# Kernel optimization log

Hardware: AMD Instinct MI355X
Metric: run time of the kernel (lower is better)

## Reference

```python
import jax, jax.numpy as jnp
import numpy as np
from jax import lax

N = 2; C_IN = 256
H0, W0 = 100, 152
H1, W1 = 50, 76
DYN_CH = 34            # 4 init_offset + 4 bound_pt_offset + 18 semantic_pt_offset + 8 reg_aggr_attn
REG_CH = 4             # 4 boundary points x 1 channel each
NUM_CLASSES = 80
SEM_PTS = 9
CLS_CH = SEM_PTS * NUM_CLASSES
BOUND_PTS = 4
RATIO = 0.5            # LIMIT_BOUND_POINT_OFFSET_RATIO

_BASE = np.array([[1,0,0,0],[0,1,0,0],[0.5,0,0.5,0],
                  [0,0.5,0,0.5],[0,0,1,0],[0,0,0,1]], np.float32)
BOUND_MAT = jnp.asarray(_BASE[[0,3,2,1,4,3,2,5]])                      # (8,4) box -> cross-shaped 4 pts
SEM_MAT = jnp.asarray(_BASE[[0,1,0,3,0,5,2,1,2,3,2,5,4,1,4,3,4,5]])    # (18,4) box -> 3x3 pts
BOUND_OFF_IDX = jnp.array([1, 2, 5, 6])   # tangential coordinate channel of each boundary point
LOC_IDX = jnp.array([0, 3, 4, 7])         # box-side coordinate channel of each boundary point

def conv3x3(x, w, b):
    y = lax.conv_general_dilated(x, w, (1, 1), 'SAME',
                                 dimension_numbers=('NCHW', 'OIHW', 'NCHW'))
    return y + b[None, :, None, None]

def conv1x1(x, w):
    return jnp.einsum('oi,nihw->nohw', w[:, :, 0, 0], x)

def pred_collect(fmap, pts, point_num, reduce_points, bias=None):
    # Bilinearly sample per-point channel groups of fmap at dynamic point locations.
    # fmap: (N, P*c, Hm, Wm); pts: (N, 2P, H, W) with (x, y) pairs per point.
    Nb, C, Hm, Wm = fmap.shape
    P = point_num; c = C // P
    H, W = pts.shape[2], pts.shape[3]
    fm = fmap.reshape(Nb, P, c, Hm, Wm)
    pg = pts.reshape(Nb, P, 2, H, W)
    def sample(f, pt):  # f: (c, Hm, Wm), pt: (2, H, W)
        x = jnp.clip(pt[0], 0.0, Wm - 1.0)
        y = jnp.clip(pt[1], 0.0, Hm - 1.0)
        x0 = jnp.floor(x); y0 = jnp.floor(y)
        fx = x - x0; fy = y - y0
        x0i = x0.astype(jnp.int32); y0i = y0.astype(jnp.int32)
        x1i = jnp.minimum(x0i + 1, Wm - 1); y1i = jnp.minimum(y0i + 1, Hm - 1)
        v00 = f[:, y0i, x0i]; v01 = f[:, y0i, x1i]
        v10 = f[:, y1i, x0i]; v11 = f[:, y1i, x1i]
        return v00*(1-fx)*(1-fy) + v01*fx*(1-fy) + v10*(1-fx)*fy + v11*fx*fy
    vals = jax.vmap(jax.vmap(sample))(fm, pg)  # (N, P, c, H, W)
    if reduce_points:
        out = vals.sum(axis=1)
        if bias is not None:
            out = out + bias[None, :, None, None]
        return out
    return vals.reshape(Nb, P * c, H, W)

def head_forward(reg_feats, cls_feats, anchors, dyn_w, dyn_b, reg_w, cls_w, cls_b):
    reg_maps = [conv1x1(x, reg_w) for x in reg_feats]
    cls_maps = [conv1x1(x, cls_w) for x in cls_feats]
    cls_scores, coarse_boxes, reg_boxes = [], [], []
    for i, (reg_feat, anchor) in enumerate(zip(reg_feats, anchors)):
        Nb, _, H, W = reg_feat.shape
        pred = conv3x3(reg_feat, dyn_w, dyn_b)
        init_off, bpt_off, spt_off, attn = jnp.split(pred, [4, 8, 26], axis=1)
        coarse = anchor + init_off                                  # (N,4,H,W) = (x1,y1,x2,y2)
        # straight-through clamp of boundary-point tangential offsets to +-wh/2*ratio
        bpt_off = bpt_off.reshape(Nb, 2, 2, 1, H, W)
        wh = jnp.stack([coarse[:, 3] - coarse[:, 1],
                        coarse[:, 2] - coarse[:, 0]], axis=1) / 2 * RATIO  # (N,2,H,W) [h,w]
        thres = wh[:, None, :, None]                                # (N,1,2,1,H,W)
        extra = jnp.maximum(bpt_off - thres, 0.0) + jnp.minimum(bpt_off + thres, 0.0)
        bpt_off = (bpt_off - lax.stop_gradient(extra)).reshape(Nb, 4, H, W)
        bound_pt = lax.stop_gradient(jnp.einsum('oc,nchw->nohw', BOUND_MAT, coarse))
        bound_pt = bound_pt.at[:, BOUND_OFF_IDX].add(bpt_off)       # (N,8,H,W)
        bound_pt_loc = bound_pt[:, LOC_IDX]                         # (N,4,H,W)
        reg_val = pred_collect(reg_maps[i], bound_pt, BOUND_PTS, False)  # (N,4,H,W)
        if i > 0:
            attn_sm = jax.nn.softmax(attn.reshape(Nb, BOUND_PTS, 2, H, W), axis=2)
            reg_hi = reg_val.reshape(Nb, BOUND_PTS, 1, 1, H, W)
            reg_lo = pred_collect(reg_maps[i - 1], bound_pt * 2, BOUND_PTS, False)
            reg_lo = reg_lo.reshape(Nb, BOUND_PTS, 1, 1, H, W) * 0.5
            reg_val = (jnp.concatenate([reg_lo, reg_hi], axis=2)
                       * attn_sm[:, :, :, None]).sum(axis=2).reshape(Nb, -1, H, W)
        reg_box = (lax.stop_gradient(bound_pt_loc) + reg_val).reshape(Nb, 4, -1, H, W).mean(axis=2)
        sem_pt = lax.stop_gradient(jnp.einsum('oc,nchw->nohw', SEM_MAT, coarse)) + spt_off
        cls_score = pred_collect(cls_maps[i], sem_pt, SEM_PTS, True, cls_b)  # (N,80,H,W)
        cls_scores.append(cls_score); coarse_boxes.append(coarse); reg_boxes.append(reg_box)
    return cls_scores, coarse_boxes, reg_boxes

def make_anchor(H, W):
    gy, gx = jnp.meshgrid(jnp.arange(H, dtype=jnp.float32),
                          jnp.arange(W, dtype=jnp.float32), indexing='ij')
    a = jnp.stack([gx - 4.0, gy - 4.0, gx + 4.0, gy + 4.0], axis=0)
    return jnp.broadcast_to(a[None], (N, 4, H, W))

def setup_inputs() -> dict:
    key = jax.random.key(0)
    ks = jax.random.split(key, 7)
    return {
        "reg_feat0": jax.random.normal(ks[0], (N, C_IN, H0, W0), jnp.float32),
        "reg_feat1": jax.random.normal(ks[1], (N, C_IN, H1, W1), jnp.float32),
        "cls_feat0": jax.random.normal(ks[2], (N, C_IN, H0, W0), jnp.float32),
        "cls_feat1": jax.random.normal(ks[3], (N, C_IN, H1, W1), jnp.float32),
        "anchor0": make_anchor(H0, W0),
        "anchor1": make_anchor(H1, W1),
        "dyn_w": jax.random.normal(ks[4], (DYN_CH, C_IN, 3, 3), jnp.float32) * 0.01,
        "dyn_b": jnp.zeros((DYN_CH,), jnp.float32),
        "reg_w": jax.random.normal(ks[5], (REG_CH, C_IN, 1, 1), jnp.float32) * 0.05,
        "cls_w": jax.random.normal(ks[6], (CLS_CH, C_IN, 1, 1), jnp.float32) * 0.05,
        "cls_b": jnp.zeros((NUM_CLASSES,), jnp.float32),
    }

def reference(reg_feat0, reg_feat1, cls_feat0, cls_feat1, anchor0, anchor1,
              dyn_w, dyn_b, reg_w, cls_w, cls_b):
    cls_scores, coarse_boxes, reg_boxes = head_forward(
        [reg_feat0, reg_feat1], [cls_feat0, cls_feat1], [anchor0, anchor1],
        dyn_w, dyn_b, reg_w, cls_w, cls_b)
    return (*cls_scores, *coarse_boxes, *reg_boxes)
```

## Files before the change

kernel.cpp:

```cpp
#include <hip/hip_runtime.h>
#include <hip/hip_bf16.h>
#include <cstdint>

#define N_BATCH 2
#define C_IN 256
#define DYN_CH 34
#define CLS_CH 720
#define NUM_CLASSES 80
#define NCOMB 48

#define P0c 15200
#define P1c 3800
#define M0c 30400
#define M1c 7600
#define MT0c 119
#define MT1c 30
#define CT0c 475
#define CT1c 119

typedef __attribute__((ext_vector_type(8))) short short8;
typedef __attribute__((ext_vector_type(4))) float f32x4;

typedef const unsigned int __attribute__((address_space(1)))* gas1_t;
typedef unsigned int __attribute__((address_space(3)))* las3_t;

__device__ __forceinline__ void async_ld16(const void* g, void* l) {
  __builtin_amdgcn_global_load_lds((gas1_t)g, (las3_t)l, 16, 0, 0);
}

__global__ __launch_bounds__(256) void pack_feat(
    const float* __restrict__ cls0, const float* __restrict__ cls1,
    const float* __restrict__ reg0, const float* __restrict__ reg1,
    const float* __restrict__ cls_w, const float* __restrict__ dyn_w,
    const float* __restrict__ reg_w, __hip_bfloat16* __restrict__ a0,
    __hip_bfloat16* __restrict__ a1, __hip_bfloat16* __restrict__ r0,
    __hip_bfloat16* __restrict__ r1, __hip_bfloat16* __restrict__ bpack,
    __hip_bfloat16* __restrict__ wpack) {
  int b = blockIdx.x;
  if (b >= 2384) {
    b -= 2384;
    if (b < 90) {
      int u = b * 256 + threadIdx.x;
      if (u >= 9 * 32 * 80) return;
      int ntile = u / 2560;
      int rem = u % 2560;
      int kcg = rem / 80;
      int ochl = rem % 80;
      int och = ntile * 80 + ochl;
      const float* wr = cls_w + (size_t)och * C_IN + kcg * 8;
      __hip_bfloat16 tmp[8];
#pragma unroll
      for (int c = 0; c < 8; ++c) tmp[c] = __float2bfloat16(wr[c]);
      *(uint4*)(bpack + (size_t)u * 8) = *(const uint4*)tmp;
    } else {
      int u = (b - 90) * 256 + threadIdx.x;
      if (u >= 13824) return;
      int j = u / 768;
      int r = u % 768;
      int n = r / 16;
      int s = r % 16;
      int ku = j * 16 + (s ^ (n & 7));
      int k0 = ku * 8;
      int tap = k0 >> 8;
      int c0 = k0 & 255;
      __hip_bfloat16 tmp[8];
#pragma unroll
      for (int i = 0; i < 8; ++i) {
        int c = c0 + i;
        float v = 0.f;
        if (n < DYN_CH) v = dyn_w[((size_t)n * C_IN + c) * 9 + tap];
        else if (n < DYN_CH + 4 && tap == 4)
          v = reg_w[(size_t)(n - DYN_CH) * C_IN + c];
        tmp[i] = __float2bfloat16(v);
      }
      *(uint4*)(wpack + (size_t)u * 8) = *(const uint4*)tmp;
    }
    return;
  }
  int j = b & 7;
  int mtg = b >> 3;
  const float* src;
  __hip_bfloat16* dst;
  int P, Mtot, mtile;
  if (mtg < 119)      { src = cls0; dst = a0; P = P0c; Mtot = M0c; mtile = mtg; }
  else if (mtg < 149) { src = cls1; dst = a1; P = P1c; Mtot = M1c; mtile = mtg - 119; }
  else if (mtg < 268) { src = reg0; dst = r0; P = P0c; Mtot = M0c; mtile = mtg - 149; }
  else                { src = reg1; dst = r1; P = P1c; Mtot = M1c; mtile = mtg - 268; }
  int wave = threadIdx.x >> 6;
  int lane = threadIdx.x & 63;
  int kcg = j * 4 + wave;
  int c0 = kcg * 8;
  int m4 = mtile * 256 + lane * 4;
  uint4* du = (uint4*)dst + (size_t)mtile * 8192 + (size_t)kcg * 256 + lane * 4;
  if (m4 < Mtot) {
    int n = m4 / P;
    int p = m4 - n * P;
    const float* sp = src + ((size_t)n * C_IN + c0) * P + p;
    float4 f[8];
#pragma unroll
    for (int c = 0; c < 8; ++c) f[c] = *(const float4*)(sp + (size_t)c * P);
#pragma unroll
    for (int i = 0; i < 4; ++i) {
      union { uint4 u; __hip_bfloat16 h[8]; } o;
#pragma unroll
      for (int c = 0; c < 8; ++c) {
        float v = (i == 0) ? f[c].x : (i == 1) ? f[c].y : (i == 2) ? f[c].z : f[c].w;
        o.h[c] = __float2bfloat16(v);
      }
      du[i] = o.u;
    }
  } else {
    uint4 z = {0u, 0u, 0u, 0u};
#pragma unroll
    for (int i = 0; i < 4; ++i) du[i] = z;
  }
}

__global__ __launch_bounds__(512) void cls_gemm_mfma(
    const uint4* __restrict__ Ap0, const uint4* __restrict__ Ap1,
    const uint4* __restrict__ Bp, __hip_bfloat16* __restrict__ out0,
    __hip_bfloat16* __restrict__ out1) {
  __shared__ uint4 Bsh[2560];
  int bb = blockIdx.x;
  int g = bb & 7;
  int loc = bb >> 3;
  int lm = loc / 9;
  int ntile = loc - lm * 9;
  int mtile = g * 19 + lm;
  if (mtile >= MT0c + MT1c) return;
  int tid = threadIdx.x;
  int w = tid >> 6;
  int lane = tid & 63;
  int l15 = lane & 15;
  int kq = lane >> 4;

  const uint4* Ap;
  __hip_bfloat16* out;
  int Mtot;
  if (mtile < MT0c) { Ap = Ap0; out = out0; Mtot = M0c; }
  else              { mtile -= MT0c; Ap = Ap1; out = out1; Mtot = M1c; }

  const uint4* Ab = Ap + (size_t)mtile * 8192;
  const uint4* Bb = Bp + (size_t)ntile * 2560;

#pragma unroll
  for (int i = 0; i < 5; ++i)
    async_ld16(Bb + i * 512 + w * 64 + lane, &Bsh[i * 512 + w * 64]);
  __syncthreads();

  f32x4 acc[2][5];
#pragma unroll
  for (int i = 0; i < 2; ++i)
#pragma unroll
    for (int j = 0; j < 5; ++j) acc[i][j] = (f32x4)0.f;

  const uint4* Abase = Ab + kq * 256 + w * 32 + l15;
#pragma unroll 2
  for (int kb = 0; kb < 8; ++kb) {
    uint4 a[2];
#pragma unroll
    for (int mi = 0; mi < 2; ++mi) a[mi] = Abase[kb * 1024 + mi * 16];
    short8 b[5];
    const uint4* Br = &Bsh[kb * 320 + kq * 80 + l15];
#pragma unroll
    for (int ni = 0; ni < 5; ++ni) b[ni] = *(const short8*)&Br[ni * 16];
#pragma unroll
    for (int mi = 0; mi < 2; ++mi)
#pragma unroll
      for (int ni = 0; ni < 5; ++ni)
        acc[mi][ni] = __builtin_amdgcn_mfma_f32_16x16x32_bf16(
            b[ni], *(const short8*)&a[mi], acc[mi][ni], 0, 0, 0);
  }

  int gbase = mtile * 256 + w * 32;
#pragma unroll
  for (int mi = 0; mi < 2; ++mi) {
    int px = gbase + mi * 16 + l15;
    if (px >= Mtot) continue;
    __hip_bfloat16* orow = out + (size_t)px * CLS_CH + ntile * 80 + kq * 4;
#pragma unroll
    for (int ni = 0; ni < 5; ++ni) {
      union { uint2 u; __hip_bfloat16 h[4]; } o;
#pragma unroll
      for (int r = 0; r < 4; ++r) o.h[r] = __float2bfloat16(acc[mi][ni][r]);
      *(uint2*)(orow + ni * 16) = o.u;
    }
  }
}

__global__ __launch_bounds__(256) void dyn_reg_conv_mfma(
    const uint4* __restrict__ rp0, const uint4* __restrict__ rp1,
    const uint4* __restrict__ wp, float* __restrict__ part0,
    float* __restrict__ part1) {
  __shared__ uint4 Bs[768];
  int g = blockIdx.x & 7;
  int i = blockIdx.x >> 3;
  int cnt = 74 + (g < 2 ? 1 : 0);
  if (i >= cnt) return;
  int bx = g * 74 + (g < 2 ? g : 2) + i;
  int tid = threadIdx.x;
  int wave = tid >> 6;
  int lane = tid & 63;
  int l15 = lane & 15;
  int kq = lane >> 4;

  const uint4* rp;
  float* part;
  int Mtot, P, W, H;
  if (bx < CT0c) { rp = rp0; part = part0; Mtot = M0c; P = P0c; W = 152; H = 100; }
  else { bx -= CT0c; rp = rp1; part = part1; Mtot = M1c; P = P1c; W = 76; H = 50; }

  int m = bx * 64 + wave * 16 + l15;
  bool mval = (m < Mtot);
  int mc = mval ? m : 0;
  int n = mc / P;
  int rem = mc - n * P;
  int y = rem / W;
  int x = rem - y * W;

  f32x4 acc[3];
#pragma unroll
  for (int q = 0; q < 3; ++q) acc[q] = (f32x4)0.f;

  for (int j = 0; j < 18; ++j) {
    const uint4* wsrc = wp + (size_t)j * 768 + wave * 192;
#pragma unroll
    for (int q = 0; q < 3; ++q)
      async_ld16(wsrc + q * 64 + lane, &Bs[wave * 192 + q * 64]);

    int tap = j >> 1;
    int cb8 = (j & 1) * 16;
    int dy = tap / 3 - 1, dx = tap % 3 - 1;
    int sy = y + dy, sx = x + dx;
    bool val = mval && ((unsigned)sy < (unsigned)H) && ((unsigned)sx < (unsigned)W);
    int sm = m + dy * W + dx;
    int smc = val ? sm : 0;
    size_t tbase = (size_t)(smc >> 8) * 8192 + (smc & 255);
    uint4 a[4];
#pragma unroll
    for (int t = 0; t < 4; ++t) {
      uint4 v = {0u, 0u, 0u, 0u};
      if (val) v = rp[tbase + (size_t)(cb8 + t * 4 + kq) * 256];
      a[t] = v;
    }
    __syncthreads();
#pragma unroll
    for (int t = 0; t < 4; ++t) {
#pragma unroll
      for (int ni = 0; ni < 3; ++ni) {
        int nn = ni * 16 + l15;
        short8 bf = *(const short8*)&Bs[nn * 16 + ((t * 4 + kq) ^ (nn & 7))];
        acc[ni] = __builtin_amdgcn_mfma_f32_16x16x32_bf16(
            *(short8*)&a[t], bf, acc[ni], 0, 0, 0);
      }
    }
    __syncthreads();
  }

  int mrow = bx * 64 + wave * 16 + kq * 4;
#pragma unroll
  for (int r = 0; r < 4; ++r) {
    int mm = mrow + r;
    if (mm >= Mtot) continue;
    float* dst = part + (size_t)mm * NCOMB + l15;
#pragma unroll
    for (int ni = 0; ni < 3; ++ni) dst[ni * 16] = acc[ni][r];
  }
}

__device__ __forceinline__ float samp(const float* __restrict__ part,
                                      int nbase, int W, int H,
                                      float px, float py, int ch) {
  float xc = fminf(fmaxf(px, 0.f), (float)(W - 1));
  float yc = fminf(fmaxf(py, 0.f), (float)(H - 1));
  float x0f = floorf(xc), y0f = floorf(yc);
  float fx = xc - x0f, fy = yc - y0f;
  int x0 = (int)x0f, y0 = (int)y0f;
  int x1 = min(x0 + 1, W - 1), y1 = min(y0 + 1, H - 1);
  float v00 = part[(size_t)(nbase + y0 * W + x0) * NCOMB + ch];
  float v01 = part[(size_t)(nbase + y0 * W + x1) * NCOMB + ch];
  float v10 = part[(size_t)(nbase + y1 * W + x0) * NCOMB + ch];
  float v11 = part[(size_t)(nbase + y1 * W + x1) * NCOMB + ch];
  return v00 * (1.f - fx) * (1.f - fy) + v01 * fx * (1.f - fy) +
         v10 * (1.f - fx) * fy + v11 * fx * fy;
}

__global__ __launch_bounds__(64) void decode(
    const float* __restrict__ part0, const float* __restrict__ part1,
    const float* __restrict__ dyn_b, const float* __restrict__ anchor0,
    const float* __restrict__ anchor1, float* __restrict__ out_coarse0,
    float* __restrict__ out_coarse1, float* __restrict__ out_regbox0,
    float* __restrict__ out_regbox1, int4* __restrict__ sidx0,
    float4* __restrict__ swt0, int4* __restrict__ sidx1,
    float4* __restrict__ swt1) {
  int g = blockIdx.x & 7;
  int i = blockIdx.x >> 3;
  int cnt = 74 + (g < 2 ? 1 : 0);
  if (i >= cnt) return;
  int u = g * 74 + (g < 2 ? g : 2) + i;
  const float* part;
  const float* anchor;
  float* out_coarse;
  float* out_regbox;
  int4* sidx;
  float4* swt;
  int Mtot, H, W, P, level, m;
  if (u < 475) {
    part = part0; anchor = anchor0; out_coarse = out_coarse0;
    out_regbox = out_regbox0; sidx = sidx0; swt = swt0;
    Mtot = M0c; H = 100; W = 152; P = P0c; level = 0;
    m = u * 64 + threadIdx.x;
  } else {
    part = part1; anchor = anchor1; out_coarse = out_coarse1;
    out_regbox = out_regbox1; sidx = sidx1; swt = swt1;
    Mtot = M1c; H = 50; W = 76; P = P1c; level = 1;
    m = (u - 475) * 64 + threadIdx.x;
  }
  if (m >= Mtot) return;
  int n = m / P;
  int p = m - n * P;
  float pr[40];
  {
    const float4* q0 = (const float4*)(part + (size_t)m * NCOMB);
#pragma unroll
    for (int o4 = 0; o4 < 10; ++o4) {
      float4 a = q0[o4];
      pr[4 * o4 + 0] = a.x;
      pr[4 * o4 + 1] = a.y;
      pr[4 * o4 + 2] = a.z;
      pr[4 * o4 + 3] = a.w;
    }
#pragma unroll
    for (int o = 0; o < DYN_CH; ++o) pr[o] += dyn_b[o];
  }
  const float* an = anchor + (size_t)n * 4 * P + p;
  float cb[4];
#pragma unroll
  for (int k = 0; k < 4; ++k) cb[k] = an[(size_t)k * P] + pr[k];
  float* oc = out_coarse + (size_t)n * 4 * P + p;
#pragma unroll
  for (int k = 0; k < 4; ++k) oc[(size_t)k * P] = cb[k];

  float thr_y = (cb[3] - cb[1]) * 0.25f;
  float thr_x = (cb[2] - cb[0]) * 0.25f;
  float bo[4];
#pragma unroll
  for (int j = 0; j < 4; ++j) {
    float thr = (j & 1) ? thr_x : thr_y;
    float b = pr[4 + j];
    float extra = fmaxf(b - thr, 0.f) + fminf(b + thr, 0.f);
    bo[j] = b - extra;
  }
  float cx = 0.5f * (cb[0] + cb[2]);
  float cy = 0.5f * (cb[1] + cb[3]);
  float bp[8] = {cb[0], cy + bo[0], cx + bo[1], cb[1],
                 cb[2], cy + bo[2], cx + bo[3], cb[3]};

  int nbase = n * P;
  int nbaseLo = n * P0c;
  float rb[4];
#pragma unroll
  for (int pt = 0; pt < 4; ++pt) {
    float hi = samp(part, nbase, W, H, bp[2 * pt], bp[2 * pt + 1],
                    DYN_CH + pt);
    float val;
    if (level == 0) {
      val = hi;
    } else {
      float lo = 0.5f * samp(part0, nbaseLo, 152, 100, bp[2 * pt] * 2.f,
                             bp[2 * pt + 1] * 2.f, DYN_CH + pt);
      float e0 = pr[26 + 2 * pt], e1 = pr[26 + 2 * pt + 1];
      float mx = fmaxf(e0, e1);
      float w0 = expf(e0 - mx), w1 = expf(e1 - mx);
      val = (lo * w0 + hi * w1) / (w0 + w1);
    }
    rb[pt] = val;
  }
  float* orb = out_regbox + (size_t)n * 4 * P + p;
  orb[0] = bp[0] + rb[0];
  orb[(size_t)P] = bp[3] + rb[1];
  orb[(size_t)2 * P] = bp[4] + rb[2];
  orb[(size_t)3 * P] = bp[7] + rb[3];

  float sx[9] = {cb[0], cb[0], cb[0], cx, cx, cx, cb[2], cb[2], cb[2]};
  float sy[9] = {cb[1], cy, cb[3], cb[1], cy, cb[3], cb[1], cy, cb[3]};
#pragma unroll
  for (int k = 0; k < 9; ++k) {
    float px = sx[k] + pr[8 + 2 * k];
    float py = sy[k] + pr[8 + 2 * k + 1];
    float xc = fminf(fmaxf(px, 0.f), (float)(W - 1));
    float yc = fminf(fmaxf(py, 0.f), (float)(H - 1));
    float x0f = floorf(xc), y0f = floorf(yc);
    float fx = xc - x0f, fy = yc - y0f;
    int x0 = (int)x0f, y0 = (int)y0f;
    int x1 = min(x0 + 1, W - 1), y1 = min(y0 + 1, H - 1);
    int4 iv;
    iv.x = (nbase + y0 * W + x0) * CLS_CH + k * 80;
    iv.y = (x1 - x0) * CLS_CH;
    iv.z = (y1 - y0) * W * CLS_CH;
    iv.w = 0;
    sidx[(size_t)k * Mtot + m] = iv;
    float4 wv = {(1.f - fx) * (1.f - fy), fx * (1.f - fy), (1.f - fx) * fy,
                 fx * fy};
    swt[(size_t)k * Mtot + m] = wv;
  }
}

__global__ __launch_bounds__(256) void cls_gather_f(
    const __hip_bfloat16* __restrict__ map0,
    const __hip_bfloat16* __restrict__ map1, const int4* __restrict__ sidx0,
    const float4* __restrict__ swt0, const int4* __restrict__ sidx1,
    const float4* __restrict__ swt1, const float* __restrict__ bias,
    float* __restrict__ outc0, float* __restrict__ outc1) {
  __shared__ float lds[NUM_CLASSES * 5];
  int b = (blockIdx.x & 7) * 1188 + (blockIdx.x >> 3);
  if (b >= 9500) return;
  const __hip_bfloat16* map;
  const int4* sidx;
  const float4* swt;
  float* out;
  int Mtot, P;
  if (b < 7600) { map = map0; sidx = sidx0; swt = swt0; out = outc0; Mtot = M0c; P = P0c; }
  else { b -= 7600; map = map1; sidx = sidx1; swt = swt1; out = outc1; Mtot = M1c; P = P1c; }
  int lane = threadIdx.x & 63;
  int wv = threadIdx.x >> 6;
  int m = b * 4 + wv;

  int sub = lane / 20;
  if (sub > 2) sub = 2;
  int cl = lane % 20;
  int c4 = cl * 4;

  float a0 = 0.f, a1 = 0.f, a2 = 0.f, a3 = 0.f;
#pragma unroll
  for (int g = 0; g < 3; ++g) {
    int pt = g * 3 + sub;
    int4 iv = sidx[(size_t)pt * Mtot + m];
    float4 wt = swt[(size_t)pt * Mtot + m];
    const __hip_bfloat16* pl = map + iv.x + c4;
    uint2 t00 = *(const uint2*)(pl);
    uint2 t01 = *(const uint2*)(pl + iv.y);
    uint2 t10 = *(const uint2*)(pl + iv.z);
    uint2 t11 = *(const uint2*)(pl + iv.y + iv.z);
    a0 += wt.x * __uint_as_float(t00.x << 16) +
          wt.y * __uint_as_float(t01.x << 16) +
          wt.z * __uint_as_float(t10.x << 16) +
          wt.w * __uint_as_float(t11.x << 16);
    a1 += wt.x * __uint_as_float(t00.x & 0xffff0000u) +
          wt.y * __uint_as_float(t01.x & 0xffff0000u) +
          wt.z * __uint_as_float(t10.x & 0xffff0000u) +
          wt.w * __uint_as_float(t11.x & 0xffff0000u);
    a2 += wt.x * __uint_as_float(t00.y << 16) +
          wt.y * __uint_as_float(t01.y << 16) +
          wt.z * __uint_as_float(t10.y << 16) +
          wt.w * __uint_as_float(t11.y << 16);
    a3 += wt.x * __uint_as_float(t00.y & 0xffff0000u) +
          wt.y * __uint_as_float(t01.y & 0xffff0000u) +
          wt.z * __uint_as_float(t10.y & 0xffff0000u) +
          wt.w * __uint_as_float(t11.y & 0xffff0000u);
  }
  {
    float s0 = __shfl(a0, lane + 20), u0 = __shfl(a0, lane + 40);
    float s1 = __shfl(a1, lane + 20), u1 = __shfl(a1, lane + 40);
    float s2 = __shfl(a2, lane + 20), u2 = __shfl(a2, lane + 40);
    float s3 = __shfl(a3, lane + 20), u3 = __shfl(a3, lane + 40);
    a0 += s0 + u0;
    a1 += s1 + u1;
    a2 += s2 + u2;
    a3 += s3 + u3;
  }
  if (lane < 20) {
    lds[(c4 + 0) * 5 + wv] = a0;
    lds[(c4 + 1) * 5 + wv] = a1;
    lds[(c4 + 2) * 5 + wv] = a2;
    lds[(c4 + 3) * 5 + wv] = a3;
  }
  __syncthreads();
  int tid = threadIdx.x;
  if (tid < NUM_CLASSES) {
    float bb = bias[tid];
    float4 v = {lds[tid * 5] + bb, lds[tid * 5 + 1] + bb, lds[tid * 5 + 2] + bb,
                lds[tid * 5 + 3] + bb};
    int m0 = b * 4;
    int n = m0 / P;
    int p0 = m0 - n * P;
    *(float4*)&out[((size_t)n * NUM_CLASSES + tid) * P + p0] = v;
  }
}

extern "C" void kernel_launch(void* const* d_in, const int* in_sizes, int n_in,
                              void* d_out, int out_size, void* d_ws,
                              size_t ws_size, hipStream_t stream) {
  const float* reg_feat0 = (const float*)d_in[0];
  const float* reg_feat1 = (const float*)d_in[1];
  const float* cls_feat0 = (const float*)d_in[2];
  const float* cls_feat1 = (const float*)d_in[3];
  const float* anchor0 = (const float*)d_in[4];
  const float* anchor1 = (const float*)d_in[5];
  const float* dyn_w = (const float*)d_in[6];
  const float* dyn_b = (const float*)d_in[7];
  const float* reg_w = (const float*)d_in[8];
  const float* cls_w = (const float*)d_in[9];
  const float* cls_b = (const float*)d_in[10];

  float* out = (float*)d_out;
  float* out_cls0 = out;
  float* out_cls1 = out_cls0 + (size_t)N_BATCH * NUM_CLASSES * P0c;
  float* out_coarse0 = out_cls1 + (size_t)N_BATCH * NUM_CLASSES * P1c;
  float* out_coarse1 = out_coarse0 + (size_t)N_BATCH * 4 * P0c;
  float* out_reg0 = out_coarse1 + (size_t)N_BATCH * 4 * P1c;
  float* out_reg1 = out_reg0 + (size_t)N_BATCH * 4 * P0c;

  char* w = (char*)d_ws;
  __hip_bfloat16* bpack = (__hip_bfloat16*)w;   w += 368640;
  __hip_bfloat16* wpack = (__hip_bfloat16*)w;   w += 221184;
  char* apack_base = w;
  __hip_bfloat16* apack0 = (__hip_bfloat16*)w;  w += 15597568;
  __hip_bfloat16* apack1 = (__hip_bfloat16*)w;  w += 3932160;
  char* rpack_base = w;
  __hip_bfloat16* rpack0 = (__hip_bfloat16*)w;  w += 15597568;
  __hip_bfloat16* rpack1 = (__hip_bfloat16*)w;  w += 3932160;
  float* part1 = (float*)w;                     w += 1459200;
  __hip_bfloat16* map0 = (__hip_bfloat16*)w;    w += 43776000;
  __hip_bfloat16* map1 = (__hip_bfloat16*)w;    w += 10944000;
  float* part0 = (float*)apack_base;
  int4* sidx0 = (int4*)rpack_base;
  float4* swt0 = (float4*)(rpack_base + 4377600);
  int4* sidx1 = (int4*)(rpack_base + 8755200);
  float4* swt1 = (float4*)(rpack_base + 9849600);

  hipLaunchKernelGGL(pack_feat, dim3(2528), dim3(256), 0, stream, cls_feat0,
                     cls_feat1, reg_feat0, reg_feat1, cls_w, dyn_w, reg_w,
                     apack0, apack1, rpack0, rpack1, bpack, wpack);
  hipLaunchKernelGGL(cls_gemm_mfma, dim3(8 * 19 * 9), dim3(512), 0, stream,
                     (const uint4*)apack0, (const uint4*)apack1,
                     (const uint4*)bpack, map0, map1);
  hipLaunchKernelGGL(dyn_reg_conv_mfma, dim3(600), dim3(256), 0,
                     stream, (const uint4*)rpack0, (const uint4*)rpack1,
                     (const uint4*)wpack, part0, part1);
  hipLaunchKernelGGL(decode, dim3(600), dim3(64), 0, stream, part0,
                     part1, dyn_b, anchor0, anchor1, out_coarse0, out_coarse1,
                     out_reg0, out_reg1, sidx0, swt0, sidx1, swt1);
  hipLaunchKernelGGL(cls_gather_f, dim3(9504), dim3(256), 0, stream, map0,
                     map1, sidx0, swt0, sidx1, swt1, cls_b, out_cls0, out_cls1);
}
```

Measured before the change: 223.4 us.

## Merge cls GEMM and decode into one launch after the dynamic conv

The classification GEMM and the decode step now run in one kernel. Extra blocks at the end of the grid run decode, with each 512-thread block handling eight 64-pixel decode units, one per wave. The dynamic conv kernel is moved ahead of it so the conv's partial sums are ready. part0 gets its own workspace region instead of aliasing the packed cls features, since the GEMM still reads those while decode runs. The goal is to save one launch and overlap the small decode work with the GEMM. The cost is a larger workspace, and decode blocks inherit the GEMM's 512-thread, shared-memory-heavy footprint.

```diff
diff --git a/kernel.cpp b/kernel.cpp
--- a/kernel.cpp
+++ b/kernel.cpp
@@ -116,78 +116,6 @@
   }
 }
 
-__global__ __launch_bounds__(512) void cls_gemm_mfma(
-    const uint4* __restrict__ Ap0, const uint4* __restrict__ Ap1,
-    const uint4* __restrict__ Bp, __hip_bfloat16* __restrict__ out0,
-    __hip_bfloat16* __restrict__ out1) {
-  __shared__ uint4 Bsh[2560];
-  int bb = blockIdx.x;
-  int g = bb & 7;
-  int loc = bb >> 3;
-  int lm = loc / 9;
-  int ntile = loc - lm * 9;
-  int mtile = g * 19 + lm;
-  if (mtile >= MT0c + MT1c) return;
-  int tid = threadIdx.x;
-  int w = tid >> 6;
-  int lane = tid & 63;
-  int l15 = lane & 15;
-  int kq = lane >> 4;
-
-  const uint4* Ap;
-  __hip_bfloat16* out;
-  int Mtot;
-  if (mtile < MT0c) { Ap = Ap0; out = out0; Mtot = M0c; }
-  else              { mtile -= MT0c; Ap = Ap1; out = out1; Mtot = M1c; }
-
-  const uint4* Ab = Ap + (size_t)mtile * 8192;
-  const uint4* Bb = Bp + (size_t)ntile * 2560;
-
-#pragma unroll
-  for (int i = 0; i < 5; ++i)
-    async_ld16(Bb + i * 512 + w * 64 + lane, &Bsh[i * 512 + w * 64]);
-  __syncthreads();
-
-  f32x4 acc[2][5];
-#pragma unroll
-  for (int i = 0; i < 2; ++i)
-#pragma unroll
-    for (int j = 0; j < 5; ++j) acc[i][j] = (f32x4)0.f;
-
-  const uint4* Abase = Ab + kq * 256 + w * 32 + l15;
-#pragma unroll 2
-  for (int kb = 0; kb < 8; ++kb) {
-    uint4 a[2];
-#pragma unroll
-    for (int mi = 0; mi < 2; ++mi) a[mi] = Abase[kb * 1024 + mi * 16];
-    short8 b[5];
-    const uint4* Br = &Bsh[kb * 320 + kq * 80 + l15];
-#pragma unroll
-    for (int ni = 0; ni < 5; ++ni) b[ni] = *(const short8*)&Br[ni * 16];
-#pragma unroll
-    for (int mi = 0; mi < 2; ++mi)
-#pragma unroll
-      for (int ni = 0; ni < 5; ++ni)
-        acc[mi][ni] = __builtin_amdgcn_mfma_f32_16x16x32_bf16(
-            b[ni], *(const short8*)&a[mi], acc[mi][ni], 0, 0, 0);
-  }
-
-  int gbase = mtile * 256 + w * 32;
-#pragma unroll
-  for (int mi = 0; mi < 2; ++mi) {
-    int px = gbase + mi * 16 + l15;
-    if (px >= Mtot) continue;
-    __hip_bfloat16* orow = out + (size_t)px * CLS_CH + ntile * 80 + kq * 4;
-#pragma unroll
-    for (int ni = 0; ni < 5; ++ni) {
-      union { uint2 u; __hip_bfloat16 h[4]; } o;
-#pragma unroll
-      for (int r = 0; r < 4; ++r) o.h[r] = __float2bfloat16(acc[mi][ni][r]);
-      *(uint2*)(orow + ni * 16) = o.u;
-    }
-  }
-}
-
 __global__ __launch_bounds__(256) void dyn_reg_conv_mfma(
     const uint4* __restrict__ rp0, const uint4* __restrict__ rp1,
     const uint4* __restrict__ wp, float* __restrict__ part0,
@@ -285,19 +213,14 @@
          v10 * (1.f - fx) * fy + v11 * fx * fy;
 }
 
-__global__ __launch_bounds__(64) void decode(
-    const float* __restrict__ part0, const float* __restrict__ part1,
-    const float* __restrict__ dyn_b, const float* __restrict__ anchor0,
-    const float* __restrict__ anchor1, float* __restrict__ out_coarse0,
-    float* __restrict__ out_coarse1, float* __restrict__ out_regbox0,
-    float* __restrict__ out_regbox1, int4* __restrict__ sidx0,
-    float4* __restrict__ swt0, int4* __restrict__ sidx1,
-    float4* __restrict__ swt1) {
-  int g = blockIdx.x & 7;
-  int i = blockIdx.x >> 3;
-  int cnt = 74 + (g < 2 ? 1 : 0);
-  if (i >= cnt) return;
-  int u = g * 74 + (g < 2 ? g : 2) + i;
+__device__ __forceinline__ void decode_unit(
+    int u, int lane, const float* __restrict__ part0,
+    const float* __restrict__ part1, const float* __restrict__ dyn_b,
+    const float* __restrict__ anchor0, const float* __restrict__ anchor1,
+    float* __restrict__ out_coarse0, float* __restrict__ out_coarse1,
+    float* __restrict__ out_regbox0, float* __restrict__ out_regbox1,
+    int4* __restrict__ sidx0, float4* __restrict__ swt0,
+    int4* __restrict__ sidx1, float4* __restrict__ swt1) {
   const float* part;
   const float* anchor;
   float* out_coarse;
@@ -309,12 +232,12 @@
     part = part0; anchor = anchor0; out_coarse = out_coarse0;
     out_regbox = out_regbox0; sidx = sidx0; swt = swt0;
     Mtot = M0c; H = 100; W = 152; P = P0c; level = 0;
-    m = u * 64 + threadIdx.x;
+    m = u * 64 + lane;
   } else {
     part = part1; anchor = anchor1; out_coarse = out_coarse1;
     out_regbox = out_regbox1; sidx = sidx1; swt = swt1;
     Mtot = M1c; H = 50; W = 76; P = P1c; level = 1;
-    m = (u - 475) * 64 + threadIdx.x;
+    m = (u - 475) * 64 + lane;
   }
   if (m >= Mtot) return;
   int n = m / P;
@@ -403,6 +326,99 @@
     float4 wv = {(1.f - fx) * (1.f - fy), fx * (1.f - fy), (1.f - fx) * fy,
                  fx * fy};
     swt[(size_t)k * Mtot + m] = wv;
+  }
+}
+
+__global__ __launch_bounds__(512) void gemm_decode_fused(
+    const uint4* __restrict__ Ap0, const uint4* __restrict__ Ap1,
+    const uint4* __restrict__ Bp, __hip_bfloat16* __restrict__ out0,
+    __hip_bfloat16* __restrict__ out1, const float* __restrict__ part0,
+    const float* __restrict__ part1, const float* __restrict__ dyn_b,
+    const float* __restrict__ anchor0, const float* __restrict__ anchor1,
+    float* __restrict__ out_coarse0, float* __restrict__ out_coarse1,
+    float* __restrict__ out_regbox0, float* __restrict__ out_regbox1,
+    int4* __restrict__ sidx0, float4* __restrict__ swt0,
+    int4* __restrict__ sidx1, float4* __restrict__ swt1) {
+  __shared__ uint4 Bsh[2560];
+  int tid = threadIdx.x;
+  int w = tid >> 6;
+  int lane = tid & 63;
+
+  if (blockIdx.x >= 1368) {
+    int d = blockIdx.x - 1368;
+    int g = d & 7;
+    int ii = d >> 3;
+    int cnt = 74 + (g < 2 ? 1 : 0);
+    int ul = ii * 8 + w;
+    if (ul >= cnt) return;
+    int u = g * 74 + (g < 2 ? g : 2) + ul;
+    decode_unit(u, lane, part0, part1, dyn_b, anchor0, anchor1, out_coarse0,
+                out_coarse1, out_regbox0, out_regbox1, sidx0, swt0, sidx1,
+                swt1);
+    return;
+  }
+
+  int bb = blockIdx.x;
+  int g = bb & 7;
+  int loc = bb >> 3;
+  int lm = loc / 9;
+  int ntile = loc - lm * 9;
+  int mtile = g * 19 + lm;
+  if (mtile >= MT0c + MT1c) return;
+  int l15 = lane & 15;
+  int kq = lane >> 4;
+
+  const uint4* Ap;
+  __hip_bfloat16* out;
+  int Mtot;
+  if (mtile < MT0c) { Ap = Ap0; out = out0; Mtot = M0c; }
+  else              { mtile -= MT0c; Ap = Ap1; out = out1; Mtot = M1c; }
+
+  const uint4* Ab = Ap + (size_t)mtile * 8192;
+  const uint4* Bb = Bp + (size_t)ntile * 2560;
+
+#pragma unroll
+  for (int i = 0; i < 5; ++i)
+    async_ld16(Bb + i * 512 + w * 64 + lane, &Bsh[i * 512 + w * 64]);
+  __syncthreads();
+
+  f32x4 acc[2][5];
+#pragma unroll
+  for (int i = 0; i < 2; ++i)
+#pragma unroll
+    for (int j = 0; j < 5; ++j) acc[i][j] = (f32x4)0.f;
+
+  const uint4* Abase = Ab + kq * 256 + w * 32 + l15;
+#pragma unroll 2
+  for (int kb = 0; kb < 8; ++kb) {
+    uint4 a[2];
+#pragma unroll
+    for (int mi = 0; mi < 2; ++mi) a[mi] = Abase[kb * 1024 + mi * 16];
+    short8 b[5];
+    const uint4* Br = &Bsh[kb * 320 + kq * 80 + l15];
+#pragma unroll
+    for (int ni = 0; ni < 5; ++ni) b[ni] = *(const short8*)&Br[ni * 16];
+#pragma unroll
+    for (int mi = 0; mi < 2; ++mi)
+#pragma unroll
+      for (int ni = 0; ni < 5; ++ni)
+        acc[mi][ni] = __builtin_amdgcn_mfma_f32_16x16x32_bf16(
+            b[ni], *(const short8*)&a[mi], acc[mi][ni], 0, 0, 0);
+  }
+
+  int gbase = mtile * 256 + w * 32;
+#pragma unroll
+  for (int mi = 0; mi < 2; ++mi) {
+    int px = gbase + mi * 16 + l15;
+    if (px >= Mtot) continue;
+    __hip_bfloat16* orow = out + (size_t)px * CLS_CH + ntile * 80 + kq * 4;
+#pragma unroll
+    for (int ni = 0; ni < 5; ++ni) {
+      union { uint2 u; __hip_bfloat16 h[4]; } o;
+#pragma unroll
+      for (int r = 0; r < 4; ++r) o.h[r] = __float2bfloat16(acc[mi][ni][r]);
+      *(uint2*)(orow + ni * 16) = o.u;
+    }
   }
 }
 
@@ -514,7 +530,6 @@
   char* w = (char*)d_ws;
   __hip_bfloat16* bpack = (__hip_bfloat16*)w;   w += 368640;
   __hip_bfloat16* wpack = (__hip_bfloat16*)w;   w += 221184;
-  char* apack_base = w;
   __hip_bfloat16* apack0 = (__hip_bfloat16*)w;  w += 15597568;
   __hip_bfloat16* apack1 = (__hip_bfloat16*)w;  w += 3932160;
   char* rpack_base = w;
@@ -523,7 +538,7 @@
   float* part1 = (float*)w;                     w += 1459200;
   __hip_bfloat16* map0 = (__hip_bfloat16*)w;    w += 43776000;
   __hip_bfloat16* map1 = (__hip_bfloat16*)w;    w += 10944000;
-  float* part0 = (float*)apack_base;
+  float* part0 = (float*)w;                     w += 5836800;
   int4* sidx0 = (int4*)rpack_base;
   float4* swt0 = (float4*)(rpack_base + 4377600);
   int4* sidx1 = (int4*)(rpack_base + 8755200);
@@ -532,15 +547,14 @@
   hipLaunchKernelGGL(pack_feat, dim3(2528), dim3(256), 0, stream, cls_feat0,
                      cls_feat1, reg_feat0, reg_feat1, cls_w, dyn_w, reg_w,
                      apack0, apack1, rpack0, rpack1, bpack, wpack);
-  hipLaunchKernelGGL(cls_gemm_mfma, dim3(8 * 19 * 9), dim3(512), 0, stream,
-                     (const uint4*)apack0, (const uint4*)apack1,
-                     (const uint4*)bpack, map0, map1);
   hipLaunchKernelGGL(dyn_reg_conv_mfma, dim3(600), dim3(256), 0,
                      stream, (const uint4*)rpack0, (const uint4*)rpack1,
                      (const uint4*)wpack, part0, part1);
-  hipLaunchKernelGGL(decode, dim3(600), dim3(64), 0, stream, part0,
-                     part1, dyn_b, anchor0, anchor1, out_coarse0, out_coarse1,
-                     out_reg0, out_reg1, sidx0, swt0, sidx1, swt1);
+  hipLaunchKernelGGL(gemm_decode_fused, dim3(1448), dim3(512), 0, stream,
+                     (const uint4*)apack0, (const uint4*)apack1,
+                     (const uint4*)bpack, map0, map1, part0, part1, dyn_b,
+                     anchor0, anchor1, out_coarse0, out_coarse1, out_reg0,
+                     out_reg1, sidx0, swt0, sidx1, swt1);
   hipLaunchKernelGGL(cls_gather_f, dim3(9504), dim3(256), 0, stream, map0,
                      map1, sidx0, swt0, sidx1, swt1, cls_b, out_cls0, out_cls1);
 }
```

Result: faster. 217.4 us (-2.7%).

## Fuse decode and class gather into one kernel using LDS sample tables

Applied to the files above, without the earlier changes.

Merges the decode kernel and the classification bilinear-gather kernel. Each block of 256 threads has one wave decode 64 pixels and write the sampling indices and weights into LDS, then all four waves gather the 9-point class features for those pixels. Output is staged in LDS so the class scores can be stored with float4 writes. This removes a kernel launch and the global round trip of the sidx/swt tables, but it cuts the gather grid from 9504 blocks to 600, leaves three waves idle during decode, and puts part0 in its own workspace region.

```diff
diff --git a/kernel.cpp b/kernel.cpp
--- a/kernel.cpp
+++ b/kernel.cpp
@@ -285,206 +285,204 @@
          v10 * (1.f - fx) * fy + v11 * fx * fy;
 }
 
-__global__ __launch_bounds__(64) void decode(
+__global__ __launch_bounds__(256) void decode_gather(
     const float* __restrict__ part0, const float* __restrict__ part1,
     const float* __restrict__ dyn_b, const float* __restrict__ anchor0,
-    const float* __restrict__ anchor1, float* __restrict__ out_coarse0,
-    float* __restrict__ out_coarse1, float* __restrict__ out_regbox0,
-    float* __restrict__ out_regbox1, int4* __restrict__ sidx0,
-    float4* __restrict__ swt0, int4* __restrict__ sidx1,
-    float4* __restrict__ swt1) {
+    const float* __restrict__ anchor1,
+    const __hip_bfloat16* __restrict__ map0,
+    const __hip_bfloat16* __restrict__ map1, const float* __restrict__ bias,
+    float* __restrict__ out_coarse0, float* __restrict__ out_coarse1,
+    float* __restrict__ out_regbox0, float* __restrict__ out_regbox1,
+    float* __restrict__ outc0, float* __restrict__ outc1) {
+  __shared__ int4 s_idx[9][64];
+  __shared__ float4 s_wt[9][64];
+  __shared__ float s_out[80][65];
   int g = blockIdx.x & 7;
-  int i = blockIdx.x >> 3;
+  int ib = blockIdx.x >> 3;
   int cnt = 74 + (g < 2 ? 1 : 0);
-  if (i >= cnt) return;
-  int u = g * 74 + (g < 2 ? g : 2) + i;
+  if (ib >= cnt) return;
+  int u = g * 74 + (g < 2 ? g : 2) + ib;
+
   const float* part;
   const float* anchor;
   float* out_coarse;
   float* out_regbox;
-  int4* sidx;
-  float4* swt;
-  int Mtot, H, W, P, level, m;
+  const __hip_bfloat16* map;
+  float* outc;
+  int Mtot, H, W, P, level, mbase;
   if (u < 475) {
     part = part0; anchor = anchor0; out_coarse = out_coarse0;
-    out_regbox = out_regbox0; sidx = sidx0; swt = swt0;
-    Mtot = M0c; H = 100; W = 152; P = P0c; level = 0;
-    m = u * 64 + threadIdx.x;
+    out_regbox = out_regbox0; map = map0; outc = outc0;
+    Mtot = M0c; H = 100; W = 152; P = P0c; level = 0; mbase = u * 64;
   } else {
     part = part1; anchor = anchor1; out_coarse = out_coarse1;
-    out_regbox = out_regbox1; sidx = sidx1; swt = swt1;
-    Mtot = M1c; H = 50; W = 76; P = P1c; level = 1;
-    m = (u - 475) * 64 + threadIdx.x;
-  }
-  if (m >= Mtot) return;
-  int n = m / P;
-  int p = m - n * P;
-  float pr[40];
-  {
-    const float4* q0 = (const float4*)(part + (size_t)m * NCOMB);
-#pragma unroll
-    for (int o4 = 0; o4 < 10; ++o4) {
-      float4 a = q0[o4];
-      pr[4 * o4 + 0] = a.x;
-      pr[4 * o4 + 1] = a.y;
-      pr[4 * o4 + 2] = a.z;
-      pr[4 * o4 + 3] = a.w;
-    }
-#pragma unroll
-    for (int o = 0; o < DYN_CH; ++o) pr[o] += dyn_b[o];
-  }
-  const float* an = anchor + (size_t)n * 4 * P + p;
-  float cb[4];
-#pragma unroll
-  for (int k = 0; k < 4; ++k) cb[k] = an[(size_t)k * P] + pr[k];
-  float* oc = out_coarse + (size_t)n * 4 * P + p;
-#pragma unroll
-  for (int k = 0; k < 4; ++k) oc[(size_t)k * P] = cb[k];
-
-  float thr_y = (cb[3] - cb[1]) * 0.25f;
-  float thr_x = (cb[2] - cb[0]) * 0.25f;
-  float bo[4];
-#pragma unroll
-  for (int j = 0; j < 4; ++j) {
-    float thr = (j & 1) ? thr_x : thr_y;
-    float b = pr[4 + j];
-    float extra = fmaxf(b - thr, 0.f) + fminf(b + thr, 0.f);
-    bo[j] = b - extra;
-  }
-  float cx = 0.5f * (cb[0] + cb[2]);
-  float cy = 0.5f * (cb[1] + cb[3]);
-  float bp[8] = {cb[0], cy + bo[0], cx + bo[1], cb[1],
-                 cb[2], cy + bo[2], cx + bo[3], cb[3]};
-
-  int nbase = n * P;
-  int nbaseLo = n * P0c;
-  float rb[4];
-#pragma unroll
-  for (int pt = 0; pt < 4; ++pt) {
-    float hi = samp(part, nbase, W, H, bp[2 * pt], bp[2 * pt + 1],
-                    DYN_CH + pt);
-    float val;
-    if (level == 0) {
-      val = hi;
-    } else {
-      float lo = 0.5f * samp(part0, nbaseLo, 152, 100, bp[2 * pt] * 2.f,
-                             bp[2 * pt + 1] * 2.f, DYN_CH + pt);
-      float e0 = pr[26 + 2 * pt], e1 = pr[26 + 2 * pt + 1];
-      float mx = fmaxf(e0, e1);
-      float w0 = expf(e0 - mx), w1 = expf(e1 - mx);
-      val = (lo * w0 + hi * w1) / (w0 + w1);
-    }
-    rb[pt] = val;
-  }
-  float* orb = out_regbox + (size_t)n * 4 * P + p;
-  orb[0] = bp[0] + rb[0];
-  orb[(size_t)P] = bp[3] + rb[1];
-  orb[(size_t)2 * P] = bp[4] + rb[2];
-  orb[(size_t)3 * P] = bp[7] + rb[3];
-
-  float sx[9] = {cb[0], cb[0], cb[0], cx, cx, cx, cb[2], cb[2], cb[2]};
-  float sy[9] = {cb[1], cy, cb[3], cb[1], cy, cb[3], cb[1], cy, cb[3]};
-#pragma unroll
-  for (int k = 0; k < 9; ++k) {
-    float px = sx[k] + pr[8 + 2 * k];
-    float py = sy[k] + pr[8 + 2 * k + 1];
-    float xc = fminf(fmaxf(px, 0.f), (float)(W - 1));
-    float yc = fminf(fmaxf(py, 0.f), (float)(H - 1));
-    float x0f = floorf(xc), y0f = floorf(yc);
-    float fx = xc - x0f, fy = yc - y0f;
-    int x0 = (int)x0f, y0 = (int)y0f;
-    int x1 = min(x0 + 1, W - 1), y1 = min(y0 + 1, H - 1);
-    int4 iv;
-    iv.x = (nbase + y0 * W + x0) * CLS_CH + k * 80;
-    iv.y = (x1 - x0) * CLS_CH;
-    iv.z = (y1 - y0) * W * CLS_CH;
-    iv.w = 0;
-    sidx[(size_t)k * Mtot + m] = iv;
-    float4 wv = {(1.f - fx) * (1.f - fy), fx * (1.f - fy), (1.f - fx) * fy,
-                 fx * fy};
-    swt[(size_t)k * Mtot + m] = wv;
-  }
-}
-
-__global__ __launch_bounds__(256) void cls_gather_f(
-    const __hip_bfloat16* __restrict__ map0,
-    const __hip_bfloat16* __restrict__ map1, const int4* __restrict__ sidx0,
-    const float4* __restrict__ swt0, const int4* __restrict__ sidx1,
-    const float4* __restrict__ swt1, const float* __restrict__ bias,
-    float* __restrict__ outc0, float* __restrict__ outc1) {
-  __shared__ float lds[NUM_CLASSES * 5];
-  int b = (blockIdx.x & 7) * 1188 + (blockIdx.x >> 3);
-  if (b >= 9500) return;
-  const __hip_bfloat16* map;
-  const int4* sidx;
-  const float4* swt;
-  float* out;
-  int Mtot, P;
-  if (b < 7600) { map = map0; sidx = sidx0; swt = swt0; out = outc0; Mtot = M0c; P = P0c; }
-  else { b -= 7600; map = map1; sidx = sidx1; swt = swt1; out = outc1; Mtot = M1c; P = P1c; }
-  int lane = threadIdx.x & 63;
-  int wv = threadIdx.x >> 6;
-  int m = b * 4 + wv;
+    out_regbox = out_regbox1; map = map1; outc = outc1;
+    Mtot = M1c; H = 50; W = 76; P = P1c; level = 1; mbase = (u - 475) * 64;
+  }
+  int tid = threadIdx.x;
+  int wv = tid >> 6;
+  int lane = tid & 63;
+
+  if (wv == 0) {
+    int m = mbase + lane;
+    if (m < Mtot) {
+      int n = m / P;
+      int p = m - n * P;
+      float pr[40];
+      {
+        const float4* q0 = (const float4*)(part + (size_t)m * NCOMB);
+#pragma unroll
+        for (int o4 = 0; o4 < 10; ++o4) {
+          float4 a = q0[o4];
+          pr[4 * o4 + 0] = a.x;
+          pr[4 * o4 + 1] = a.y;
+          pr[4 * o4 + 2] = a.z;
+          pr[4 * o4 + 3] = a.w;
+        }
+#pragma unroll
+        for (int o = 0; o < DYN_CH; ++o) pr[o] += dyn_b[o];
+      }
+      const float* an = anchor + (size_t)n * 4 * P + p;
+      float cb[4];
+#pragma unroll
+      for (int k = 0; k < 4; ++k) cb[k] = an[(size_t)k * P] + pr[k];
+      float* oc = out_coarse + (size_t)n * 4 * P + p;
+#pragma unroll
+      for (int k = 0; k < 4; ++k) oc[(size_t)k * P] = cb[k];
+
+      float thr_y = (cb[3] - cb[1]) * 0.25f;
+      float thr_x = (cb[2] - cb[0]) * 0.25f;
+      float bo[4];
+#pragma unroll
+      for (int j = 0; j < 4; ++j) {
+        float thr = (j & 1) ? thr_x : thr_y;
+        float b = pr[4 + j];
+        float extra = fmaxf(b - thr, 0.f) + fminf(b + thr, 0.f);
+        bo[j] = b - extra;
+      }
+      float cx = 0.5f * (cb[0] + cb[2]);
+      float cy = 0.5f * (cb[1] + cb[3]);
+      float bp[8] = {cb[0], cy + bo[0], cx + bo[1], cb[1],
+                     cb[2], cy + bo[2], cx + bo[3], cb[3]};
+
+      int nbase = n * P;
+      int nbaseLo = n * P0c;
+      float rb[4];
+#pragma unroll
+      for (int pt = 0; pt < 4; ++pt) {
+        float hi = samp(part, nbase, W, H, bp[2 * pt], bp[2 * pt + 1],
+                        DYN_CH + pt);
+        float val;
+        if (level == 0) {
+          val = hi;
+        } else {
+          float lo = 0.5f * samp(part0, nbaseLo, 152, 100, bp[2 * pt] * 2.f,
+                                 bp[2 * pt + 1] * 2.f, DYN_CH + pt);
+          float e0 = pr[26 + 2 * pt], e1 = pr[26 + 2 * pt + 1];
+          float mx = fmaxf(e0, e1);
+          float w0 = expf(e0 - mx), w1 = expf(e1 - mx);
+          val = (lo * w0 + hi * w1) / (w0 + w1);
+        }
+        rb[pt] = val;
+      }
+      float* orb = out_regbox + (size_t)n * 4 * P + p;
+      orb[0] = bp[0] + rb[0];
+      orb[(size_t)P] = bp[3] + rb[1];
+      orb[(size_t)2 * P] = bp[4] + rb[2];
+      orb[(size_t)3 * P] = bp[7] + rb[3];
+
+      float sx[9] = {cb[0], cb[0], cb[0], cx, cx, cx, cb[2], cb[2], cb[2]};
+      float sy[9] = {cb[1], cy, cb[3], cb[1], cy, cb[3], cb[1], cy, cb[3]};
+#pragma unroll
+      for (int k = 0; k < 9; ++k) {
+        float px = sx[k] + pr[8 + 2 * k];
+        float py = sy[k] + pr[8 + 2 * k + 1];
+        float xc = fminf(fmaxf(px, 0.f), (float)(W - 1));
+        float yc = fminf(fmaxf(py, 0.f), (float)(H - 1));
+        float x0f = floorf(xc), y0f = floorf(yc);
+        float fx = xc - x0f, fy = yc - y0f;
+        int x0 = (int)x0f, y0 = (int)y0f;
+        int x1 = min(x0 + 1, W - 1), y1 = min(y0 + 1, H - 1);
+        int4 iv;
+        iv.x = (nbase + y0 * W + x0) * CLS_CH + k * 80;
+        iv.y = (x1 - x0) * CLS_CH;
+        iv.z = (y1 - y0) * W * CLS_CH;
+        iv.w = 0;
+        s_idx[k][lane] = iv;
+        float4 wv4 = {(1.f - fx) * (1.f - fy), fx * (1.f - fy),
+                      (1.f - fx) * fy, fx * fy};
+        s_wt[k][lane] = wv4;
+      }
+    }
+  }
+  __syncthreads();
 
   int sub = lane / 20;
   if (sub > 2) sub = 2;
   int cl = lane % 20;
   int c4 = cl * 4;
-
-  float a0 = 0.f, a1 = 0.f, a2 = 0.f, a3 = 0.f;
-#pragma unroll
-  for (int g = 0; g < 3; ++g) {
-    int pt = g * 3 + sub;
-    int4 iv = sidx[(size_t)pt * Mtot + m];
-    float4 wt = swt[(size_t)pt * Mtot + m];
-    const __hip_bfloat16* pl = map + iv.x + c4;
-    uint2 t00 = *(const uint2*)(pl);
-    uint2 t01 = *(const uint2*)(pl + iv.y);
-    uint2 t10 = *(const uint2*)(pl + iv.z);
-    uint2 t11 = *(const uint2*)(pl + iv.y + iv.z);
-    a0 += wt.x * __uint_as_float(t00.x << 16) +
-          wt.y * __uint_as_float(t01.x << 16) +
-          wt.z * __uint_as_float(t10.x << 16) +
-          wt.w * __uint_as_float(t11.x << 16);
-    a1 += wt.x * __uint_as_float(t00.x & 0xffff0000u) +
-          wt.y * __uint_as_float(t01.x & 0xffff0000u) +
-          wt.z * __uint_as_float(t10.x & 0xffff0000u) +
-          wt.w * __uint_as_float(t11.x & 0xffff0000u);
-    a2 += wt.x * __uint_as_float(t00.y << 16) +
-          wt.y * __uint_as_float(t01.y << 16) +
-          wt.z * __uint_as_float(t10.y << 16) +
-          wt.w * __uint_as_float(t11.y << 16);
-    a3 += wt.x * __uint_as_float(t00.y & 0xffff0000u) +
-          wt.y * __uint_as_float(t01.y & 0xffff0000u) +
-          wt.z * __uint_as_float(t10.y & 0xffff0000u) +
-          wt.w * __uint_as_float(t11.y & 0xffff0000u);
-  }
-  {
-    float s0 = __shfl(a0, lane + 20), u0 = __shfl(a0, lane + 40);
-    float s1 = __shfl(a1, lane + 20), u1 = __shfl(a1, lane + 40);
-    float s2 = __shfl(a2, lane + 20), u2 = __shfl(a2, lane + 40);
-    float s3 = __shfl(a3, lane + 20), u3 = __shfl(a3, lane + 40);
-    a0 += s0 + u0;
-    a1 += s1 + u1;
-    a2 += s2 + u2;
-    a3 += s3 + u3;
-  }
-  if (lane < 20) {
-    lds[(c4 + 0) * 5 + wv] = a0;
-    lds[(c4 + 1) * 5 + wv] = a1;
-    lds[(c4 + 2) * 5 + wv] = a2;
-    lds[(c4 + 3) * 5 + wv] = a3;
+  for (int r = 0; r < 16; ++r) {
+    int pxl = wv * 16 + r;
+    int m = mbase + pxl;
+    if (m >= Mtot) break;
+    float a0 = 0.f, a1 = 0.f, a2 = 0.f, a3 = 0.f;
+#pragma unroll
+    for (int gg = 0; gg < 3; ++gg) {
+      int pt = gg * 3 + sub;
+      int4 iv = s_idx[pt][pxl];
+      float4 wt = s_wt[pt][pxl];
+      const __hip_bfloat16* pl = map + iv.x + c4;
+      uint2 t00 = *(const uint2*)(pl);
+      uint2 t01 = *(const uint2*)(pl + iv.y);
+      uint2 t10 = *(const uint2*)(pl + iv.z);
+      uint2 t11 = *(const uint2*)(pl + iv.y + iv.z);
+      a0 += wt.x * __uint_as_float(t00.x << 16) +
+            wt.y * __uint_as_float(t01.x << 16) +
+            wt.z * __uint_as_float(t10.x << 16) +
+            wt.w * __uint_as_float(t11.x << 16);
+      a1 += wt.x * __uint_as_float(t00.x & 0xffff0000u) +
+            wt.y * __uint_as_float(t01.x & 0xffff0000u) +
+            wt.z * __uint_as_float(t10.x & 0xffff0000u) +
+            wt.w * __uint_as_float(t11.x & 0xffff0000u);
+      a2 += wt.x * __uint_as_float(t00.y << 16) +
+            wt.y * __uint_as_float(t01.y << 16) +
+            wt.z * __uint_as_float(t10.y << 16) +
+            wt.w * __uint_as_float(t11.y << 16);
+      a3 += wt.x * __uint_as_float(t00.y & 0xffff0000u) +
+            wt.y * __uint_as_float(t01.y & 0xffff0000u) +
+            wt.z * __uint_as_float(t10.y & 0xffff0000u) +
+            wt.w * __uint_as_float(t11.y & 0xffff0000u);
+    }
+    {
+      float s0 = __shfl(a0, lane + 20), u0 = __shfl(a0, lane + 40);
+      float s1 = __shfl(a1, lane + 20), u1 = __shfl(a1, lane + 40);
+      float s2 = __shfl(a2, lane + 20), u2 = __shfl(a2, lane + 40);
+      float s3 = __shfl(a3, lane + 20), u3 = __shfl(a3, lane + 40);
+      a0 += s0 + u0;
+      a1 += s1 + u1;
+      a2 += s2 + u2;
+      a3 += s3 + u3;
+    }
+    if (lane < 20) {
+      s_out[c4 + 0][pxl] = a0;
+      s_out[c4 + 1][pxl] = a1;
+      s_out[c4 + 2][pxl] = a2;
+      s_out[c4 + 3][pxl] = a3;
+    }
   }
   __syncthreads();
-  int tid = threadIdx.x;
-  if (tid < NUM_CLASSES) {
-    float bb = bias[tid];
-    float4 v = {lds[tid * 5] + bb, lds[tid * 5 + 1] + bb, lds[tid * 5 + 2] + bb,
-                lds[tid * 5 + 3] + bb};
-    int m0 = b * 4;
-    int n = m0 / P;
-    int p0 = m0 - n * P;
-    *(float4*)&out[((size_t)n * NUM_CLASSES + tid) * P + p0] = v;
+
+  for (int k = tid; k < 80 * 16; k += 256) {
+    int c = k >> 4;
+    int q = k & 15;
+    int m4 = mbase + q * 4;
+    if (m4 >= Mtot) continue;
+    int n = m4 / P;
+    int p4 = m4 - n * P;
+    float bb = bias[c];
+    float4 v = {s_out[c][q * 4 + 0] + bb, s_out[c][q * 4 + 1] + bb,
+                s_out[c][q * 4 + 2] + bb, s_out[c][q * 4 + 3] + bb};
+    *(float4*)&outc[((size_t)n * NUM_CLASSES + c) * P + p4] = v;
   }
 }
 
@@ -514,20 +512,14 @@
   char* w = (char*)d_ws;
   __hip_bfloat16* bpack = (__hip_bfloat16*)w;   w += 368640;
   __hip_bfloat16* wpack = (__hip_bfloat16*)w;   w += 221184;
-  char* apack_base = w;
   __hip_bfloat16* apack0 = (__hip_bfloat16*)w;  w += 15597568;
   __hip_bfloat16* apack1 = (__hip_bfloat16*)w;  w += 3932160;
-  char* rpack_base = w;
   __hip_bfloat16* rpack0 = (__hip_bfloat16*)w;  w += 15597568;
   __hip_bfloat16* rpack1 = (__hip_bfloat16*)w;  w += 3932160;
   float* part1 = (float*)w;                     w += 1459200;
   __hip_bfloat16* map0 = (__hip_bfloat16*)w;    w += 43776000;
   __hip_bfloat16* map1 = (__hip_bfloat16*)w;    w += 10944000;
-  float* part0 = (float*)apack_base;
-  int4* sidx0 = (int4*)rpack_base;
-  float4* swt0 = (float4*)(rpack_base + 4377600);
-  int4* sidx1 = (int4*)(rpack_base + 8755200);
-  float4* swt1 = (float4*)(rpack_base + 9849600);
+  float* part0 = (float*)w;                     w += 5836800;
 
   hipLaunchKernelGGL(pack_feat, dim3(2528), dim3(256), 0, stream, cls_feat0,
                      cls_feat1, reg_feat0, reg_feat1, cls_w, dyn_w, reg_w,
@@ -538,9 +530,8 @@
   hipLaunchKernelGGL(dyn_reg_conv_mfma, dim3(600), dim3(256), 0,
                      stream, (const uint4*)rpack0, (const uint4*)rpack1,
                      (const uint4*)wpack, part0, part1);
-  hipLaunchKernelGGL(decode, dim3(600), dim3(64), 0, stream, part0,
-                     part1, dyn_b, anchor0, anchor1, out_coarse0, out_coarse1,
-                     out_reg0, out_reg1, sidx0, swt0, sidx1, swt1);
-  hipLaunchKernelGGL(cls_gather_f, dim3(9504), dim3(256), 0, stream, map0,
-                     map1, sidx0, swt0, sidx1, swt1, cls_b, out_cls0, out_cls1);
-}
+  hipLaunchKernelGGL(decode_gather, dim3(600), dim3(256), 0, stream, part0,
+                     part1, dyn_b, anchor0, anchor1, map0, map1, cls_b,
+                     out_coarse0, out_coarse1, out_reg0, out_reg1, out_cls0,
+                     out_cls1);
+}
```

Measured after the change: 207.5 us. -7.1%, faster.
